# Kernel optimization log

Hardware: AMD Instinct MI355X
Metric: run time of the kernel (lower is better)

## Reference

```python
import jax, jax.numpy as jnp
import numpy as np

B, L, DIM = 1, 2048, 512
DHEAD = 64
HEADS = DIM // DHEAD  # 8
KS = 127              # kernel_size (odd)
EXP = 4


def setup_inputs() -> dict:
    key = jax.random.key(0)
    ks = jax.random.split(key, 8)
    sc = 0.02
    rnd = lambda k, shape: (jax.random.normal(k, shape, jnp.float32) * sc)
    return {
        "x": jax.random.normal(ks[0], (B, L, DIM), jnp.float32),
        "ln1_g": jnp.ones((DIM,), jnp.float32),
        "ln1_b": jnp.zeros((DIM,), jnp.float32),
        "qkv_w": rnd(ks[1], (DIM, 3 * DIM)),
        "qkv_b": jnp.zeros((3 * DIM,), jnp.float32),
        "rpb": rnd(ks[2], (HEADS, 2 * KS - 1)),
        "proj_w": rnd(ks[3], (DIM, DIM)),
        "proj_b": jnp.zeros((DIM,), jnp.float32),
        "ln2_g": jnp.ones((DIM,), jnp.float32),
        "ln2_b": jnp.zeros((DIM,), jnp.float32),
        "ff1_w": rnd(ks[4], (DIM, DIM * EXP)),
        "ff1_b": jnp.zeros((DIM * EXP,), jnp.float32),
        "ff2_w": rnd(ks[5], (DIM * EXP, DIM)),
        "ff2_b": jnp.zeros((DIM,), jnp.float32),
    }


def _layernorm(x, g, b, eps=1e-5):
    m = x.mean(-1, keepdims=True)
    v = ((x - m) ** 2).mean(-1, keepdims=True)
    return (x - m) * jax.lax.rsqrt(v + eps) * g + b


def _neighborhood_attn_1d(x, qkv_w, qkv_b, rpb, proj_w, proj_b):
    # NATTEN NeighborhoodAttention1D: window of KS keys per query, clamped
    # at sequence edges so every query sees exactly KS keys (requires L >= KS).
    b, l, dim = x.shape
    qkv = (x @ qkv_w + qkv_b).reshape(b, l, 3, HEADS, DHEAD)
    q, k, v = qkv[:, :, 0], qkv[:, :, 1], qkv[:, :, 2]  # [b,l,h,d]
    scale = DHEAD ** -0.5
    # window start per query, clamped to stay in-bounds
    starts = jnp.clip(jnp.arange(l) - KS // 2, 0, l - KS)          # [l]
    idx = starts[:, None] + jnp.arange(KS)                         # [l,KS]
    kg = k[:, idx]                                                 # [b,l,KS,h,d]
    vg = v[:, idx]                                                 # [b,l,KS,h,d]
    logits = jnp.einsum('blhd,blkhd->blhk', q * scale, kg)         # [b,l,h,KS]
    # relative-position bias: index = (j - i) + (KS - 1), in [0, 2KS-2]
    bias_idx = idx - jnp.arange(l)[:, None] + (KS - 1)             # [l,KS]
    logits = logits + rpb[:, bias_idx].transpose(1, 0, 2)[None]    # [1,l,h,KS]
    attn = jax.nn.softmax(logits, axis=-1)
    out = jnp.einsum('blhk,blkhd->blhd', attn, vg).reshape(b, l, dim)
    return out @ proj_w + proj_b


def reference(x, ln1_g, ln1_b, qkv_w, qkv_b, rpb, proj_w, proj_b,
              ln2_g, ln2_b, ff1_w, ff1_b, ff2_w, ff2_b):
    x = x + _neighborhood_attn_1d(_layernorm(x, ln1_g, ln1_b),
                                  qkv_w, qkv_b, rpb, proj_w, proj_b)
    h = _layernorm(x, ln2_g, ln2_b)
    h = jax.nn.gelu(h @ ff1_w + ff1_b, approximate=False) @ ff2_w + ff2_b
    return x + h
```

## Files before the change

### kernel.cpp

```cpp
#include <hip/hip_runtime.h>
#include <hip/hip_bf16.h>

static constexpr int Lc     = 2048;
static constexpr int DIMc   = 512;
static constexpr int HEADSc = 8;
static constexpr int DHEADc = 64;
static constexpr int KSc    = 127;
static constexpr int NQKVc  = 1536;

typedef __attribute__((ext_vector_type(8))) short short8;
typedef __attribute__((ext_vector_type(4))) float f32x4;
typedef unsigned short u16;
typedef unsigned int u32;

__device__ __forceinline__ float b2f(u16 s) {
  return __uint_as_float(((u32)s) << 16);
}
__device__ __forceinline__ u16 f2b(float x) {
  u32 u = __float_as_uint(x);
  return (u16)((u + 0x7fffu + ((u >> 16) & 1u)) >> 16);
}
__device__ __forceinline__ void gload16(const void* g, void* l) {
  __builtin_amdgcn_global_load_lds(
      (const __attribute__((address_space(1))) u32*)g,
      (__attribute__((address_space(3))) u32*)l, 16, 0, 0);
}

__global__ __launch_bounds__(256) void prep_kernel(
    const float* __restrict__ w0, const float* __restrict__ w1,
    const float* __restrict__ w2, const float* __restrict__ w3,
    u16* __restrict__ o0, u16* __restrict__ o1, u16* __restrict__ o2,
    u16* __restrict__ o3, const float* __restrict__ xin,
    const float* __restrict__ g, const float* __restrict__ b,
    u16* __restrict__ lnout) {
  __shared__ float tl[32][33];
  __shared__ float rs[4], rq[4], stat[2];
  const int tid = threadIdx.x;
  if (blockIdx.x >= 3072) {
    const int row = blockIdx.x - 3072;
    const float* rp = xin + (size_t)row * DIMc;
    float v0 = rp[tid];
    float v1 = rp[tid + 256];
    float s = v0 + v1;
    float sq = v0 * v0 + v1 * v1;
#pragma unroll
    for (int o = 32; o > 0; o >>= 1) {
      s += __shfl_down(s, o);
      sq += __shfl_down(sq, o);
    }
    const int wid = tid >> 6, lane = tid & 63;
    if (lane == 0) { rs[wid] = s; rq[wid] = sq; }
    __syncthreads();
    if (tid == 0) {
      float S = rs[0] + rs[1] + rs[2] + rs[3];
      float Q = rq[0] + rq[1] + rq[2] + rq[3];
      float m = S / DIMc;
      float var = Q / DIMc - m * m;
      stat[0] = m;
      stat[1] = rsqrtf(var + 1e-5f);
    }
    __syncthreads();
    const float m = stat[0], r = stat[1];
    lnout[(size_t)row * DIMc + tid] = f2b((v0 - m) * r * g[tid] + b[tid]);
    lnout[(size_t)row * DIMc + tid + 256] =
        f2b((v1 - m) * r * g[tid + 256] + b[tid + 256]);
    return;
  }
  int t = blockIdx.x;
  const float* W;
  u16* O;
  int K, N;
  if (t < 768)       { W = w0; O = o0; K = 512;  N = 1536; }
  else if (t < 1024) { W = w1; O = o1; K = 512;  N = 512;  t -= 768; }
  else if (t < 2048) { W = w2; O = o2; K = 512;  N = 2048; t -= 1024; }
  else               { W = w3; O = o3; K = 2048; N = 512;  t -= 2048; }
  const int nt = N >> 5;
  const int by = t / nt, bx = t % nt;
  const int c = tid & 31, r0 = tid >> 5;
#pragma unroll
  for (int i = 0; i < 4; ++i) {
    const int r = r0 + i * 8;
    tl[r][c] = W[(size_t)(by * 32 + r) * N + bx * 32 + c];
  }
  __syncthreads();
#pragma unroll
  for (int i = 0; i < 4; ++i) {
    const int r = r0 + i * 8;
    O[(size_t)(bx * 32 + r) * K + by * 32 + c] = f2b(tl[c][r]);
  }
}

__global__ __launch_bounds__(256) void ln2x_kernel(
    const u16* __restrict__ parts, const float* __restrict__ x,
    const float* __restrict__ pb, const float* __restrict__ g,
    const float* __restrict__ b, float* __restrict__ x2,
    u16* __restrict__ lnout) {
  const int row = blockIdx.x;
  const int tid = threadIdx.x;
  const size_t base = (size_t)row * DIMc;
  float v0, v1;
  {
    const int c0 = tid, c1 = tid + 256;
    v0 = x[base + c0] + pb[c0] + b2f(parts[base + c0]) +
         b2f(parts[(size_t)Lc * DIMc + base + c0]);
    v1 = x[base + c1] + pb[c1] + b2f(parts[base + c1]) +
         b2f(parts[(size_t)Lc * DIMc + base + c1]);
  }
  x2[base + tid] = v0;
  x2[base + tid + 256] = v1;
  float s = v0 + v1;
  float sq = v0 * v0 + v1 * v1;
  __shared__ float rs[4], rq[4], stat[2];
#pragma unroll
  for (int o = 32; o > 0; o >>= 1) {
    s += __shfl_down(s, o);
    sq += __shfl_down(sq, o);
  }
  const int wid = tid >> 6, lane = tid & 63;
  if (lane == 0) { rs[wid] = s; rq[wid] = sq; }
  __syncthreads();
  if (tid == 0) {
    float S = rs[0] + rs[1] + rs[2] + rs[3];
    float Q = rq[0] + rq[1] + rq[2] + rq[3];
    float m = S / DIMc;
    float var = Q / DIMc - m * m;
    stat[0] = m;
    stat[1] = rsqrtf(var + 1e-5f);
  }
  __syncthreads();
  const float m = stat[0], r = stat[1];
  lnout[base + tid] = f2b((v0 - m) * r * g[tid] + b[tid]);
  lnout[base + tid + 256] = f2b((v1 - m) * r * g[tid + 256] + b[tid + 256]);
}

template <int OP, int SPLIT, typename OUT_T>
__global__ __launch_bounds__(128) void mfma_gemm(
    const u16* __restrict__ A, const u16* __restrict__ Bt,
    const float* __restrict__ bias, OUT_T* __restrict__ C, int M, int N,
    int K) {
  constexpr int BK = 32;
  __shared__ __align__(16) u16 As[2][64 * BK];
  __shared__ __align__(16) u16 Bs[2][64 * BK];
  const int tid = threadIdx.x;
  const int wave = tid >> 6, lane = tid & 63;
  const int m0 = blockIdx.y * 64, n0 = blockIdx.x * 64;
  const int wn = wave * 32;
  const int z = (SPLIT > 1) ? blockIdx.z : 0;
  const int kslice = K / SPLIT;
  const int kbeg = z * kslice;
  const int T = kslice / BK;

  f32x4 acc[4][2] = {};

  const int fr = lane & 15;
  const int fk8 = (lane >> 4) * 8;

  const int srow = tid >> 2;
  const int scol = (tid & 3) * 8;
  const int ldsbase = wave * 512;

#define STAGE(k0, buf)                                                        \
  {                                                                           \
    _Pragma("unroll") for (int i = 0; i < 2; ++i) {                           \
      gload16(A + (size_t)(m0 + i * 32 + srow) * K + (k0) + scol,             \
              &As[buf][i * 1024 + ldsbase]);                                  \
      gload16(Bt + (size_t)(n0 + i * 32 + srow) * K + (k0) + scol,            \
              &Bs[buf][i * 1024 + ldsbase]);                                  \
    }                                                                         \
  }

  STAGE(kbeg, 0);
  __syncthreads();

  for (int t = 0; t < T; ++t) {
    const int cur = t & 1;
    if (t + 1 < T) STAGE(kbeg + (t + 1) * BK, cur ^ 1);

    short8 af[4], bf[2];
#pragma unroll
    for (int i = 0; i < 4; ++i)
      af[i] = *(const short8*)&As[cur][(i * 16 + fr) * BK + fk8];
#pragma unroll
    for (int j = 0; j < 2; ++j)
      bf[j] = *(const short8*)&Bs[cur][(wn + j * 16 + fr) * BK + fk8];
#pragma unroll
    for (int i = 0; i < 4; ++i)
#pragma unroll
      for (int j = 0; j < 2; ++j)
        acc[i][j] = __builtin_amdgcn_mfma_f32_16x16x32_bf16(af[i], bf[j],
                                                            acc[i][j], 0, 0, 0);
    __syncthreads();
  }
#undef STAGE

  const int cl = lane & 15;
  const int rbase = (lane >> 4) * 4;
#pragma unroll
  for (int i = 0; i < 4; ++i) {
#pragma unroll
    for (int j = 0; j < 2; ++j) {
      const int c = n0 + wn + j * 16 + cl;
      const float bv = (OP == 3) ? 0.f : bias[c];
#pragma unroll
      for (int r = 0; r < 4; ++r) {
        const int row = m0 + i * 16 + rbase + r;
        float v = acc[i][j][r] + bv;
        if (OP == 1) v = 0.5f * v * (1.0f + erff(v * 0.70710678118f));
        const size_t o = (size_t)row * N + c;
        if (OP == 3) {
          ((u16*)C)[(size_t)z * M * N + o] = f2b(v);
        } else {
          ((u16*)C)[o] = f2b(v);
        }
      }
    }
  }
}

__global__ __launch_bounds__(256) void ff2_reduce(const u16* __restrict__ part,
                                                  const float* __restrict__ x2,
                                                  const float* __restrict__ bias,
                                                  float* __restrict__ out) {
  const int i = blockIdx.x * 256 + threadIdx.x;
  const size_t b = (size_t)i * 4;
  const int col = (int)(b & (DIMc - 1));
  const float4 r = *(const float4*)(x2 + b);
  const float4 bb = *(const float4*)(bias + col);
  float4 s = {r.x + bb.x, r.y + bb.y, r.z + bb.z, r.w + bb.w};
#pragma unroll
  for (int zz = 0; zz < 4; ++zz) {
    const ushort4 p =
        *(const ushort4*)(part + (size_t)zz * (Lc * DIMc) + b);
    s.x += b2f(p.x);
    s.y += b2f(p.y);
    s.z += b2f(p.z);
    s.w += b2f(p.w);
  }
  *(float4*)(out + b) = s;
}

__global__ __launch_bounds__(256) void attn_mfma(const u16* __restrict__ qkv,
                                                 const float* __restrict__ rpb,
                                                 u16* __restrict__ out) {
  constexpr int NR = 192, NT = 12, PP = 200;
  __shared__ __align__(16) u16 Ks[NR * DHEADc];
  __shared__ __align__(16) u16 Vt[DHEADc * NR];
  __shared__ __align__(16) u16 Ps[4][16 * PP];
  __shared__ float rp[2 * KSc - 1];
  const int h = blockIdx.y, l0 = blockIdx.x * 64, tid = threadIdx.x;
  const int wv = tid >> 6, lane = tid & 63;
  const int fr = lane & 15, hi = lane >> 4;

  int s_min = l0 - 63;
  if (s_min < 0) s_min = 0;
  if (s_min > Lc - KSc) s_min = Lc - KSc;

  for (int i = tid; i < 2 * KSc - 1; i += 256) rp[i] = rpb[h * (2 * KSc - 1) + i];

#pragma unroll
  for (int rd = 0; rd < 6; ++rd) {
    const int linear = rd * 4096 + wv * 1024 + lane * 16;
    const int row = linear >> 7;
    const int seg = (linear >> 4) & 7;
    const int segp = seg ^ (row & 7);
    int gl = s_min + row;
    if (gl > Lc - 1) gl = Lc - 1;
    gload16(qkv + (size_t)gl * NQKVc + DIMc + h * DHEADc + segp * 8,
            (char*)Ks + rd * 4096 + wv * 1024);
  }

#pragma unroll
  for (int rd = 0; rd < 3; ++rd) {
    const int t = rd * 256 + tid;
    const int rpair = t >> 3, seg = t & 7;
    const int r0 = rpair * 2;
    int g0 = s_min + r0, g1 = s_min + r0 + 1;
    if (g0 > Lc - 1) g0 = Lc - 1;
    if (g1 > Lc - 1) g1 = Lc - 1;
    const short8 a =
        *(const short8*)(qkv + (size_t)g0 * NQKVc + 2 * DIMc + h * DHEADc + seg * 8);
    const short8 bq =
        *(const short8*)(qkv + (size_t)g1 * NQKVc + 2 * DIMc + h * DHEADc + seg * 8);
#pragma unroll
    for (int j = 0; j < 8; ++j) {
      const int d = seg * 8 + j;
      int byte = d * (NR * 2) + r0 * 2;
      byte ^= (d & 7) << 4;
      *(u32*)((char*)Vt + byte) =
          ((u32)(u16)a[j]) | (((u32)(u16)bq[j]) << 16);
    }
  }

  const int lq = l0 + wv * 16 + fr;
  short8 qf[2];
#pragma unroll
  for (int ks = 0; ks < 2; ++ks)
    qf[ks] = *(const short8*)(qkv + (size_t)lq * NQKVc + h * DHEADc + ks * 32 + hi * 8);

  __syncthreads();

  f32x4 S[NT] = {};
#pragma unroll
  for (int jt = 0; jt < NT; ++jt) {
#pragma unroll
    for (int ks = 0; ks < 2; ++ks) {
      int byte = (jt * 16 + fr) * 128 + ks * 64 + hi * 16;
      byte ^= (fr & 7) << 4;
      const short8 kf = *(const short8*)((const char*)Ks + byte);
      S[jt] = __builtin_amdgcn_mfma_f32_16x16x32_bf16(qf[ks], kf, S[jt], 0, 0, 0);
    }
  }

  float inv4[4];
#pragma unroll
  for (int r = 0; r < 4; ++r) {
    const int l = l0 + wv * 16 + hi * 4 + r;
    int st = l - 63;
    if (st < 0) st = 0;
    if (st > Lc - KSc) st = Lc - KSc;
    float mx = -3e38f;
#pragma unroll
    for (int jt = 0; jt < NT; ++jt) {
      const int pos = s_min + jt * 16 + fr;
      const int j = pos - st;
      float v = -3e38f;
      if (j >= 0 && j <= KSc - 1) v = S[jt][r] * 0.125f + rp[pos - l + KSc - 1];
      S[jt][r] = v;
      mx = fmaxf(mx, v);
    }
#pragma unroll
    for (int o = 1; o < 16; o <<= 1) mx = fmaxf(mx, __shfl_xor(mx, o));
    float sum = 0.f;
#pragma unroll
    for (int jt = 0; jt < NT; ++jt) {
      const float e = __expf(S[jt][r] - mx);
      S[jt][r] = e;
      sum += e;
    }
#pragma unroll
    for (int o = 1; o < 16; o <<= 1) sum += __shfl_xor(sum, o);
    inv4[r] = 1.f / sum;
  }

#pragma unroll
  for (int jt = 0; jt < NT; ++jt)
#pragma unroll
    for (int r = 0; r < 4; ++r)
      Ps[wv][(hi * 4 + r) * PP + jt * 16 + fr] = f2b(S[jt][r] * inv4[r]);

  f32x4 O[4] = {};
#pragma unroll
  for (int ks = 0; ks < 6; ++ks) {
    const short8 pa =
        *(const short8*)((const char*)Ps[wv] + fr * (PP * 2) + ks * 64 + hi * 16);
#pragma unroll
    for (int dt = 0; dt < 4; ++dt) {
      int byte = (dt * 16 + fr) * (NR * 2) + ks * 64 + hi * 16;
      byte ^= (fr & 7) << 4;
      const short8 vb = *(const short8*)((const char*)Vt + byte);
      O[dt] = __builtin_amdgcn_mfma_f32_16x16x32_bf16(pa, vb, O[dt], 0, 0, 0);
    }
  }

#pragma unroll
  for (int dt = 0; dt < 4; ++dt)
#pragma unroll
    for (int r = 0; r < 4; ++r)
      out[(size_t)(l0 + wv * 16 + hi * 4 + r) * DIMc + h * DHEADc + dt * 16 + fr] =
          f2b(O[dt][r]);
}

extern "C" void kernel_launch(void* const* d_in, const int* in_sizes, int n_in,
                              void* d_out, int out_size, void* d_ws,
                              size_t ws_size, hipStream_t stream) {
  const float* x      = (const float*)d_in[0];
  const float* ln1_g  = (const float*)d_in[1];
  const float* ln1_b  = (const float*)d_in[2];
  const float* qkv_w  = (const float*)d_in[3];
  const float* qkv_b  = (const float*)d_in[4];
  const float* rpb    = (const float*)d_in[5];
  const float* proj_w = (const float*)d_in[6];
  const float* proj_b = (const float*)d_in[7];
  const float* ln2_g  = (const float*)d_in[8];
  const float* ln2_b  = (const float*)d_in[9];
  const float* ff1_w  = (const float*)d_in[10];
  const float* ff1_b  = (const float*)d_in[11];
  const float* ff2_w  = (const float*)d_in[12];
  const float* ff2_b  = (const float*)d_in[13];
  float* out = (float*)d_out;

  char* ws = (char*)d_ws;
  u16*   lnbuf   = (u16*)(ws);
  u16*   qkvbuf  = (u16*)(ws + ((size_t)2  << 20));
  u16*   attnbuf = (u16*)(ws + ((size_t)8  << 20));
  float* x2      = (float*)(ws + ((size_t)10 << 20));
  u16*   ff1buf  = (u16*)(ws + ((size_t)14 << 20));
  u16*   wt_qkv  = (u16*)(ws + ((size_t)22 << 20));
  u16*   wt_proj = (u16*)(ws + ((size_t)23 << 20) + ((size_t)512 << 10));
  u16*   wt_ff1  = (u16*)(ws + ((size_t)24 << 20));
  u16*   wt_ff2  = (u16*)(ws + ((size_t)26 << 20));
  u16*   parts   = (u16*)(ws + ((size_t)2  << 20));

  prep_kernel<<<5120, 256, 0, stream>>>(qkv_w, proj_w, ff1_w, ff2_w, wt_qkv,
                                        wt_proj, wt_ff1, wt_ff2, x, ln1_g,
                                        ln1_b, lnbuf);
  mfma_gemm<0, 1, u16><<<dim3(NQKVc / 64, Lc / 64), 128, 0, stream>>>(
      lnbuf, wt_qkv, qkv_b, qkvbuf, Lc, NQKVc, DIMc);
  attn_mfma<<<dim3(Lc / 64, HEADSc), 256, 0, stream>>>(qkvbuf, rpb, attnbuf);
  mfma_gemm<3, 2, u16><<<dim3(DIMc / 64, Lc / 64, 2), 128, 0, stream>>>(
      attnbuf, wt_proj, nullptr, parts, Lc, DIMc, DIMc);
  ln2x_kernel<<<Lc, 256, 0, stream>>>(parts, x, proj_b, ln2_g, ln2_b, x2, lnbuf);
  mfma_gemm<1, 1, u16><<<dim3(4 * DIMc / 64, Lc / 64), 128, 0, stream>>>(
      lnbuf, wt_ff1, ff1_b, ff1buf, Lc, 4 * DIMc, DIMc);
  mfma_gemm<3, 4, u16><<<dim3(DIMc / 64, Lc / 64, 4), 128, 0, stream>>>(
      ff1buf, wt_ff2, nullptr, parts, Lc, DIMc, 4 * DIMc);
  ff2_reduce<<<(Lc * DIMc / 4) / 256, 256, 0, stream>>>(parts, x2, ff2_b, out);
}
```

Before: 79.38 us.

## Replace split-K partial buffers with fp32 atomic accumulation into residual outputs

```diff
diff --git a/kernel.cpp b/kernel.cpp
--- a/kernel.cpp
+++ b/kernel.cpp
@@ -32,15 +32,18 @@
     u16* __restrict__ o0, u16* __restrict__ o1, u16* __restrict__ o2,
     u16* __restrict__ o3, const float* __restrict__ xin,
     const float* __restrict__ g, const float* __restrict__ b,
-    u16* __restrict__ lnout) {
+    u16* __restrict__ lnout, const float* __restrict__ pb,
+    float* __restrict__ x2init) {
   __shared__ float tl[32][33];
   __shared__ float rs[4], rq[4], stat[2];
   const int tid = threadIdx.x;
   if (blockIdx.x >= 3072) {
     const int row = blockIdx.x - 3072;
-    const float* rp = xin + (size_t)row * DIMc;
-    float v0 = rp[tid];
-    float v1 = rp[tid + 256];
+    const size_t base = (size_t)row * DIMc;
+    float v0 = xin[base + tid];
+    float v1 = xin[base + tid + 256];
+    x2init[base + tid] = v0 + pb[tid];
+    x2init[base + tid + 256] = v1 + pb[tid + 256];
     float s = v0 + v1;
     float sq = v0 * v0 + v1 * v1;
 #pragma unroll
@@ -61,8 +64,8 @@
     }
     __syncthreads();
     const float m = stat[0], r = stat[1];
-    lnout[(size_t)row * DIMc + tid] = f2b((v0 - m) * r * g[tid] + b[tid]);
-    lnout[(size_t)row * DIMc + tid + 256] =
+    lnout[base + tid] = f2b((v0 - m) * r * g[tid] + b[tid]);
+    lnout[base + tid + 256] =
         f2b((v1 - m) * r * g[tid + 256] + b[tid + 256]);
     return;
   }
@@ -90,24 +93,17 @@
   }
 }
 
-__global__ __launch_bounds__(256) void ln2x_kernel(
-    const u16* __restrict__ parts, const float* __restrict__ x,
-    const float* __restrict__ pb, const float* __restrict__ g,
-    const float* __restrict__ b, float* __restrict__ x2,
-    u16* __restrict__ lnout) {
+__global__ __launch_bounds__(256) void ln2o_kernel(
+    const float* __restrict__ x2, const float* __restrict__ g,
+    const float* __restrict__ b, const float* __restrict__ fb,
+    u16* __restrict__ lnout, float* __restrict__ outp) {
   const int row = blockIdx.x;
   const int tid = threadIdx.x;
   const size_t base = (size_t)row * DIMc;
-  float v0, v1;
-  {
-    const int c0 = tid, c1 = tid + 256;
-    v0 = x[base + c0] + pb[c0] + b2f(parts[base + c0]) +
-         b2f(parts[(size_t)Lc * DIMc + base + c0]);
-    v1 = x[base + c1] + pb[c1] + b2f(parts[base + c1]) +
-         b2f(parts[(size_t)Lc * DIMc + base + c1]);
-  }
-  x2[base + tid] = v0;
-  x2[base + tid + 256] = v1;
+  const float v0 = x2[base + tid];
+  const float v1 = x2[base + tid + 256];
+  outp[base + tid] = v0 + fb[tid];
+  outp[base + tid + 256] = v1 + fb[tid + 256];
   float s = v0 + v1;
   float sq = v0 * v0 + v1 * v1;
   __shared__ float rs[4], rq[4], stat[2];
@@ -200,43 +196,21 @@
 #pragma unroll
     for (int j = 0; j < 2; ++j) {
       const int c = n0 + wn + j * 16 + cl;
-      const float bv = (OP == 3) ? 0.f : bias[c];
+      const float bv = (OP == 4) ? 0.f : bias[c];
 #pragma unroll
       for (int r = 0; r < 4; ++r) {
         const int row = m0 + i * 16 + rbase + r;
         float v = acc[i][j][r] + bv;
         if (OP == 1) v = 0.5f * v * (1.0f + erff(v * 0.70710678118f));
         const size_t o = (size_t)row * N + c;
-        if (OP == 3) {
-          ((u16*)C)[(size_t)z * M * N + o] = f2b(v);
+        if (OP == 4) {
+          unsafeAtomicAdd(&((float*)C)[o], v);
         } else {
           ((u16*)C)[o] = f2b(v);
         }
       }
     }
   }
-}
-
-__global__ __launch_bounds__(256) void ff2_reduce(const u16* __restrict__ part,
-                                                  const float* __restrict__ x2,
-                                                  const float* __restrict__ bias,
-                                                  float* __restrict__ out) {
-  const int i = blockIdx.x * 256 + threadIdx.x;
-  const size_t b = (size_t)i * 4;
-  const int col = (int)(b & (DIMc - 1));
-  const float4 r = *(const float4*)(x2 + b);
-  const float4 bb = *(const float4*)(bias + col);
-  float4 s = {r.x + bb.x, r.y + bb.y, r.z + bb.z, r.w + bb.w};
-#pragma unroll
-  for (int zz = 0; zz < 4; ++zz) {
-    const ushort4 p =
-        *(const ushort4*)(part + (size_t)zz * (Lc * DIMc) + b);
-    s.x += b2f(p.x);
-    s.y += b2f(p.y);
-    s.z += b2f(p.z);
-    s.w += b2f(p.w);
-  }
-  *(float4*)(out + b) = s;
 }
 
 __global__ __launch_bounds__(256) void attn_mfma(const u16* __restrict__ qkv,
@@ -399,20 +373,18 @@
   u16*   wt_proj = (u16*)(ws + ((size_t)23 << 20) + ((size_t)512 << 10));
   u16*   wt_ff1  = (u16*)(ws + ((size_t)24 << 20));
   u16*   wt_ff2  = (u16*)(ws + ((size_t)26 << 20));
-  u16*   parts   = (u16*)(ws + ((size_t)2  << 20));
 
   prep_kernel<<<5120, 256, 0, stream>>>(qkv_w, proj_w, ff1_w, ff2_w, wt_qkv,
                                         wt_proj, wt_ff1, wt_ff2, x, ln1_g,
-                                        ln1_b, lnbuf);
+                                        ln1_b, lnbuf, proj_b, x2);
   mfma_gemm<0, 1, u16><<<dim3(NQKVc / 64, Lc / 64), 128, 0, stream>>>(
       lnbuf, wt_qkv, qkv_b, qkvbuf, Lc, NQKVc, DIMc);
   attn_mfma<<<dim3(Lc / 64, HEADSc), 256, 0, stream>>>(qkvbuf, rpb, attnbuf);
-  mfma_gemm<3, 2, u16><<<dim3(DIMc / 64, Lc / 64, 2), 128, 0, stream>>>(
-      attnbuf, wt_proj, nullptr, parts, Lc, DIMc, DIMc);
-  ln2x_kernel<<<Lc, 256, 0, stream>>>(parts, x, proj_b, ln2_g, ln2_b, x2, lnbuf);
+  mfma_gemm<4, 2, float><<<dim3(DIMc / 64, Lc / 64, 2), 128, 0, stream>>>(
+      attnbuf, wt_proj, nullptr, x2, Lc, DIMc, DIMc);
+  ln2o_kernel<<<Lc, 256, 0, stream>>>(x2, ln2_g, ln2_b, ff2_b, lnbuf, out);
   mfma_gemm<1, 1, u16><<<dim3(4 * DIMc / 64, Lc / 64), 128, 0, stream>>>(
       lnbuf, wt_ff1, ff1_b, ff1buf, Lc, 4 * DIMc, DIMc);
-  mfma_gemm<3, 4, u16><<<dim3(DIMc / 64, Lc / 64, 4), 128, 0, stream>>>(
-      ff1buf, wt_ff2, nullptr, parts, Lc, DIMc, 4 * DIMc);
-  ff2_reduce<<<(Lc * DIMc / 4) / 256, 256, 0, stream>>>(parts, x2, ff2_b, out);
-}
+  mfma_gemm<4, 4, float><<<dim3(DIMc / 64, Lc / 64, 4), 128, 0, stream>>>(
+      ff1buf, wt_ff2, nullptr, out, Lc, DIMc, 4 * DIMc);
+}
```

New measurement: 86.71 us. 9.2% more time.
